# Optimization experiments

Measured on AMD Instinct MI355X. Metric: run time of the kernel, lower is better.

The kernel has to match this reference:

```python
import jax, jax.numpy as jnp
import numpy as np

B, N, D_FEAT = 16, 4096, 64
NPOINT, NSAMPLE = 1024, 32
MLP = [64, 64, 128]
IN_CH = 3 + D_FEAT
EPS = 1e-5  # BatchNorm eps (torch default)


def _fps(xyz, npoint):
    # Farthest point sampling; sequential scan over npoint steps (matches torch loop).
    b, n, _ = xyz.shape
    def step(carry, _):
        distance, farthest = carry  # (B,N) running min dist, (B,) current centroid idx
        centroid = jnp.take_along_axis(xyz, farthest[:, None, None], axis=1)  # (B,1,3)
        d = jnp.sum((xyz - centroid) ** 2, -1)  # (B,N)
        distance = jnp.minimum(distance, d)
        nxt = jnp.argmax(distance, -1).astype(jnp.int32)
        return (distance, nxt), farthest
    init = (jnp.full((b, n), jnp.inf, dtype=xyz.dtype),
            jnp.full((b,), n // 2, dtype=jnp.int32))
    _, centroids = jax.lax.scan(step, init, None, length=npoint)
    return centroids.T  # (B, npoint)


def _gather(pts, idx):
    # pts: (B,N,C); idx: (B,...) int -> (B,...,C)
    return jax.vmap(lambda p, i: p[i])(pts, idx)


def setup_inputs() -> dict:
    key = jax.random.key(0)
    ks = jax.random.split(key, 16)
    inp = {
        'xyz': jax.random.normal(ks[0], (B, N, 3), jnp.float32),
        'points': jax.random.normal(ks[1], (B, N, D_FEAT), jnp.float32),
    }
    last = IN_CH
    for li, oc in enumerate(MLP):
        inp[f'W{li}'] = jax.random.normal(ks[2 + li], (oc, last), jnp.float32) * (1.0 / np.sqrt(last))
        inp[f'b{li}'] = jnp.zeros((oc,), jnp.float32)
        inp[f'g{li}'] = jnp.ones((oc,), jnp.float32)
        inp[f'be{li}'] = jnp.zeros((oc,), jnp.float32)
        last = oc
    C = MLP[-1]; R = C // 8
    inp['aW1'] = jax.random.normal(ks[10], (R, C), jnp.float32) * (1.0 / np.sqrt(C))
    inp['aW2'] = jax.random.normal(ks[11], (C, R), jnp.float32) * (1.0 / np.sqrt(R))
    return inp


def reference(xyz, points, W0, b0, g0, be0, W1, b1, g1, be1, W2, b2, g2, be2, aW1, aW2):
    fps_idx = _fps(xyz, NPOINT)                 # (B,S) int32
    new_xyz = _gather(xyz, fps_idx)             # (B,S,3)
    # squared distances (B,S,N) via matmul expansion (as torch square_distance)
    d = (-2.0 * jnp.einsum('bsc,bnc->bsn', new_xyz, xyz)
         + jnp.sum(new_xyz ** 2, -1)[..., None]
         + jnp.sum(xyz ** 2, -1)[:, None, :])
    _, idx = jax.lax.top_k(-d, NSAMPLE)         # (B,S,k) nearest neighbors
    grouped_xyz = _gather(xyz, idx)             # (B,S,k,3)
    rel = grouped_xyz - new_xyz[:, :, None, :]  # relative coords
    feat = _gather(points, idx)                 # (B,S,k,D)
    g = jnp.concatenate([rel, feat], axis=-1)   # (B,S,k,3+D) channels-last
    # 1x1 conv MLP + BatchNorm (training-mode batch stats) + ReLU
    for (W, b, ga, be) in ((W0, b0, g0, be0), (W1, b1, g1, be1), (W2, b2, g2, be2)):
        g = jnp.einsum('bskc,oc->bsko', g, W) + b
        mu = g.mean(axis=(0, 1, 2))
        var = g.var(axis=(0, 1, 2))
        g = ga * (g - mu) * jax.lax.rsqrt(var + EPS) + be
        g = jax.nn.relu(g)
    new_points = g.max(axis=2)                  # max over nsample -> (B,S,C)
    # channel attention on (B,C,S) == reductions over S here
    avg = new_points.mean(axis=1)               # (B,C)
    mx = new_points.max(axis=1)                 # (B,C)
    def fc(v):
        return jnp.einsum('cr,br->bc', aW2, jax.nn.relu(jnp.einsum('rc,bc->br', aW1, v)))
    scale = jax.nn.sigmoid(fc(avg) + fc(mx))    # (B,C)
    new_points = new_points * scale[:, None, :]
    return new_xyz, new_points, fps_idx
```

## Files before the change

### kernel.cpp

```cpp
#include <hip/hip_runtime.h>
#include <hip/hip_bf16.h>

#define BB 16
#define NN 4096
#define SS 1024
#define KS 32
#define DF 64
#define INC 67
#define C1 64
#define C2 64
#define C3 128
#define ROWS (BB*SS*KS)
#define EPSBN 1e-5f
#define F_INF (__builtin_inff())

typedef __bf16 bf16;
typedef __bf16 bfrag __attribute__((ext_vector_type(8)));
typedef float  ffrag __attribute__((ext_vector_type(4)));
typedef float  f2    __attribute__((ext_vector_type(2)));
typedef unsigned long long u64;

#define OUT_NXYZ 0
#define OUT_NP   49152
#define OUT_FPS  2146304

#define OFF_FPS   0u
#define OFF_NXYZ  65536u
#define OFF_IDX   262144u
#define OFF_STATS 2359296u
#define OFF_ASUM  2555904u
#define OFF_AMAX  2621440u
#define OFF_BNC   2686976u
#define OFF_SCALE 2690048u
#define OFF_NP0   2698240u
#define OFF_YMAX  11086848u
#define OFF_H1    19475456u
#define OFF_H2    86584320u
#define ZERO_BYTES (196608u + 65536u + 65536u)

#define DPP_MAX_STEP(k, ctrl, rmask, bc) { \
  int _lo = __builtin_amdgcn_update_dpp(0, (int)(unsigned)(k), (ctrl), (rmask), 0xf, (bc)); \
  int _hi = __builtin_amdgcn_update_dpp(0, (int)((k)>>32),     (ctrl), (rmask), 0xf, (bc)); \
  u64 _k2 = ((u64)(unsigned)_hi << 32) | (unsigned)_lo; \
  if (_k2 > (k)) (k) = _k2; }

#define DPP_FMAX_STEP(v, ctrl, rmask, bc) { \
  int _t = __builtin_amdgcn_update_dpp(0, __float_as_int(v), (ctrl), (rmask), 0xf, (bc)); \
  (v) = fmaxf((v), __uint_as_float((unsigned)_t)); }

__device__ __forceinline__ u64 dpp_wavemax64(u64 k){
  DPP_MAX_STEP(k, 0x111, 0xf, true)
  DPP_MAX_STEP(k, 0x112, 0xf, true)
  DPP_MAX_STEP(k, 0x114, 0xf, true)
  DPP_MAX_STEP(k, 0x118, 0xf, true)
  DPP_MAX_STEP(k, 0x142, 0xa, false)
  DPP_MAX_STEP(k, 0x143, 0xc, false)
  return k;
}

__device__ __forceinline__ u64 readlane64(u64 k, int lane){
  unsigned lo = (unsigned)__builtin_amdgcn_readlane((int)(unsigned)k, lane);
  unsigned hi = (unsigned)__builtin_amdgcn_readlane((int)(k >> 32),   lane);
  return ((u64)hi << 32) | lo;
}

__device__ __forceinline__ u64 umax64(u64 a, u64 b){ return a > b ? a : b; }

__global__ __launch_bounds__(256) void fps_kernel(const float* __restrict__ xyz,
                                                  int* __restrict__ fps_i,
                                                  float* __restrict__ nxyz_ws,
                                                  float* __restrict__ out)
{
  #pragma clang fp contract(off)
  __shared__ __align__(16) float4 lc[NN];
  __shared__ int lfps[SS];
  __shared__ __align__(16) u64 slotk[2][4];
  int b = blockIdx.x, t = threadIdx.x;
  const float* xb = xyz + (size_t)b*NN*3;
  for (int p = t; p < NN; p += 256){
    lc[p] = make_float4(xb[p*3], xb[p*3+1], xb[p*3+2], 0.f);
  }
  __syncthreads();
  f2 px2[8], py2[8], pz2[8], pd2[8];
  int p0 = t*16;
  #pragma unroll
  for (int j=0;j<8;++j){
    float4 a = lc[p0+2*j], c = lc[p0+2*j+1];
    px2[j] = (f2){a.x, c.x}; py2[j] = (f2){a.y, c.y}; pz2[j] = (f2){a.z, c.z};
    pd2[j] = (f2){F_INF, F_INF};
  }
  float cx = lc[NN/2].x, cy = lc[NN/2].y, cz = lc[NN/2].z;
  if (t==0) lfps[0]=NN/2;
  int wv = t >> 6, lane = t & 63;
  for (int it=1; it<SS; ++it){
    f2 c2x = (f2){cx,cx}, c2y = (f2){cy,cy}, c2z = (f2){cz,cz};
    float bv=-1.f; int bi=p0;
    #pragma unroll
    for (int j=0;j<8;++j){
      f2 dx = px2[j]-c2x, dy = py2[j]-c2y, dz = pz2[j]-c2z;
      f2 d = (dx*dx + dy*dy) + dz*dz;
      f2 nd = (f2){fminf(pd2[j].x, d.x), fminf(pd2[j].y, d.y)};
      pd2[j]=nd;
      if (nd.x > bv){ bv=nd.x; bi=p0+2*j; }
      if (nd.y > bv){ bv=nd.y; bi=p0+2*j+1; }
    }
    float mv = bv;
    DPP_FMAX_STEP(mv, 0x111, 0xf, true)
    DPP_FMAX_STEP(mv, 0x112, 0xf, true)
    DPP_FMAX_STEP(mv, 0x114, 0xf, true)
    DPP_FMAX_STEP(mv, 0x118, 0xf, true)
    DPP_FMAX_STEP(mv, 0x142, 0xa, false)
    DPP_FMAX_STEP(mv, 0x143, 0xc, false)
    float wmax = __uint_as_float((unsigned)__builtin_amdgcn_readlane(__float_as_int(mv), 63));
    u64 em = __ballot(bv == wmax);
    int wl = (int)__builtin_ctzll(em);
    int wbi = __builtin_amdgcn_readlane(bi, wl);
    int p = it & 1;
    if (lane == 0)
      slotk[p][wv] = ((u64)__float_as_uint(wmax) << 32) | (unsigned)(~wbi);
    __syncthreads();
    ulonglong2 sA = *(const ulonglong2*)&slotk[p][0];
    ulonglong2 sB = *(const ulonglong2*)&slotk[p][2];
    u64 k = umax64(umax64(sA.x, sA.y), umax64(sB.x, sB.y));
    int i = ~(unsigned)k;
    float4 cc = lc[i];
    cx = cc.x; cy = cc.y; cz = cc.z;
    if (t==0) lfps[it]=i;
  }
  __syncthreads();
  for (int s=t; s<SS; s+=256){
    int i = lfps[s];
    fps_i[b*SS+s]=i;
    out[OUT_FPS + b*SS + s] = (float)i;
    float4 cc = lc[i];
    int o3 = (b*SS+s)*3;
    out[OUT_NXYZ+o3]=cc.x; out[OUT_NXYZ+o3+1]=cc.y; out[OUT_NXYZ+o3+2]=cc.z;
    nxyz_ws[o3]=cc.x; nxyz_ws[o3+1]=cc.y; nxyz_ws[o3+2]=cc.z;
  }
}

__global__ __launch_bounds__(64) void knn_kernel(const float* __restrict__ xyz,
                                                 const float* __restrict__ nxyz,
                                                 int* __restrict__ knn)
{
  __shared__ float ld[NN];
  int lane = threadIdx.x;
  int bs = blockIdx.x;
  int b = bs >> 10;
  const float* xb = xyz + (size_t)b*NN*3;
  float sx=nxyz[bs*3], sy=nxyz[bs*3+1], sz=nxyz[bs*3+2];
  float gv[8]; int gi[8];
  float lv = F_INF; int li = 0;
  #pragma unroll
  for (int g=0; g<8; ++g){
    float bgv = F_INF; int bgi = 0;
    #pragma unroll
    for (int jj=0; jj<8; ++jj){
      int p = (g*8+jj)*64 + lane;
      float dx=xb[p*3]-sx, dy=xb[p*3+1]-sy, dz=xb[p*3+2]-sz;
      float d = dx*dx+dy*dy+dz*dz;
      ld[p] = d;
      if (d < bgv){ bgv=d; bgi=p; }
    }
    gv[g]=bgv; gi[g]=bgi;
    if (bgv < lv){ lv=bgv; li=bgi; }
  }
  int kept = 0;
  for (int it=0; it<KS; ++it){
    u64 mk = ~(((u64)__float_as_uint(lv) << 32) | (unsigned)li);
    mk = dpp_wavemax64(mk);
    mk = readlane64(mk, 63);
    int i = (int)(unsigned)(~mk);
    if (lane==it) kept = i;
    if ((i & 63) == lane){
      int j = i >> 6;
      ld[i] = F_INF;
      int g = j >> 3;
      float bgv=F_INF; int bgi=0;
      for (int jj=0;jj<8;++jj){
        int p = (g*8+jj)*64 + lane;
        float d = ld[p];
        if (d<bgv){bgv=d;bgi=p;}
      }
      #pragma unroll
      for (int q=0;q<8;++q){ if (q==g){ gv[q]=bgv; gi[q]=bgi; } }
      lv=F_INF; li=0;
      #pragma unroll
      for (int q=0;q<8;++q){ if (gv[q]<lv){ lv=gv[q]; li=gi[q]; } }
    }
  }
  if (lane < KS) knn[bs*KS + lane] = kept;
}

__global__ __launch_bounds__(256) void conv1_kernel(const float* __restrict__ xyz,
                                                    const float* __restrict__ points,
                                                    const float* __restrict__ W0,
                                                    const float* __restrict__ b0,
                                                    const float* __restrict__ nxyz,
                                                    const int* __restrict__ knn,
                                                    bf16* __restrict__ h1,
                                                    float* __restrict__ stats)
{
  __shared__ __align__(16) bf16 As[64][104];
  __shared__ __align__(16) bf16 Bs[64][104];
  __shared__ float s1[C1], s2[C1];
  int t = threadIdx.x;
  int Rbase = blockIdx.x * 64;
  if (t < C1){ s1[t]=0.f; s2[t]=0.f; }
  {
    int o = t >> 2, q = t & 3;
    const float* wr = W0 + o*INC;
    for (int cc = q*24; cc < q*24+24; ++cc){
      float w;
      if (cc < 64) w = wr[3+cc];
      else if (cc < 67) w = wr[cc-64];
      else w = 0.f;
      Bs[o][cc] = (bf16)w;
    }
  }
  {
    int r = t >> 2, q = t & 3;
    int R = Rbase + r;
    int bs = R >> 5;
    int bIdx = bs >> 10;
    int nI = knn[R];
    const float* pr = points + ((size_t)(bIdx*NN + nI))*DF + q*16;
    float4 f0 = *(const float4*)(pr);
    float4 f1 = *(const float4*)(pr+4);
    float4 f2v = *(const float4*)(pr+8);
    float4 f3 = *(const float4*)(pr+12);
    bf16* ap = &As[r][q*16];
    ap[0]=(bf16)f0.x; ap[1]=(bf16)f0.y; ap[2]=(bf16)f0.z; ap[3]=(bf16)f0.w;
    ap[4]=(bf16)f1.x; ap[5]=(bf16)f1.y; ap[6]=(bf16)f1.z; ap[7]=(bf16)f1.w;
    ap[8]=(bf16)f2v.x; ap[9]=(bf16)f2v.y; ap[10]=(bf16)f2v.z; ap[11]=(bf16)f2v.w;
    ap[12]=(bf16)f3.x; ap[13]=(bf16)f3.y; ap[14]=(bf16)f3.z; ap[15]=(bf16)f3.w;
    if (q==0){
      const float* xr = xyz + ((size_t)(bIdx*NN + nI))*3;
      const float* nr = nxyz + bs*3;
      As[r][64]=(bf16)(xr[0]-nr[0]);
      As[r][65]=(bf16)(xr[1]-nr[1]);
      As[r][66]=(bf16)(xr[2]-nr[2]);
      for (int cc=67; cc<96; ++cc) As[r][cc]=(bf16)0.f;
    }
  }
  __syncthreads();
  int wv = t >> 6, lane = t & 63;
  int row16 = wv * 16;
  int arow = lane & 15, kgrp = lane >> 4;
  ffrag acc[4] = {};
  #pragma unroll
  for (int kc = 0; kc < 3; ++kc){
    bfrag af = *(const bfrag*)&As[row16 + arow][kc*32 + kgrp*8];
    #pragma unroll
    for (int nt = 0; nt < 4; ++nt){
      bfrag bfv = *(const bfrag*)&Bs[nt*16 + arow][kc*32 + kgrp*8];
      acc[nt] = __builtin_amdgcn_mfma_f32_16x16x32_bf16(af, bfv, acc[nt], 0,0,0);
    }
  }
  #pragma unroll
  for (int nt=0; nt<4; ++nt){
    int c = nt*16 + arow;
    float bias = b0[c];
    float ls1=0.f, ls2=0.f;
    #pragma unroll
    for (int r=0;r<4;++r){
      float y = acc[nt][r] + bias;
      int grow = Rbase + row16 + kgrp*4 + r;
      h1[(size_t)grow*C1 + c] = (bf16)y;
      ls1 += y; ls2 += y*y;
    }
    ls1 += __shfl_xor(ls1, 16); ls1 += __shfl_xor(ls1, 32);
    ls2 += __shfl_xor(ls2, 16); ls2 += __shfl_xor(ls2, 32);
    if (kgrp==0){ atomicAdd(&s1[c], ls1); atomicAdd(&s2[c], ls2); }
  }
  __syncthreads();
  if (t < C1){
    float* gp = stats + (blockIdx.x & 63)*256;
    atomicAdd(&gp[t], s1[t]);
    atomicAdd(&gp[128 + t], s2[t]);
  }
}

__global__ void bnfin_kernel(const float* __restrict__ stats, const float* __restrict__ g,
                             const float* __restrict__ be, float* __restrict__ bnc, int C)
{
  int c = threadIdx.x; if (c >= C) return;
  float a1=0.f, a2=0.f;
  for (int q=0;q<64;++q){ a1 += stats[q*256+c]; a2 += stats[q*256+128+c]; }
  float inv = 1.f/(float)ROWS;
  float mu = a1*inv; float var = a2*inv - mu*mu;
  float a = g[c]*rsqrtf(var + EPSBN);
  bnc[c] = a; bnc[128+c] = be[c] - mu*a;
}

__global__ __launch_bounds__(256) void conv2_kernel(const bf16* __restrict__ h1,
                                                    const float* __restrict__ W1,
                                                    const float* __restrict__ b1,
                                                    const float* __restrict__ bnc,
                                                    bf16* __restrict__ h2,
                                                    float* __restrict__ stats)
{
  __shared__ __align__(16) bf16 As[64][72];
  __shared__ __align__(16) bf16 Bs[64][72];
  __shared__ float s1[C2], s2[C2];
  int t = threadIdx.x;
  int Rbase = blockIdx.x * 64;
  if (t < C2){ s1[t]=0.f; s2[t]=0.f; }
  {
    int o = t >> 2, q = t & 3;
    const float* wr = W1 + o*64 + q*16;
    bf16* bp = &Bs[o][q*16];
    #pragma unroll
    for (int v=0; v<4; ++v){
      float4 f = *(const float4*)(wr + v*4);
      bp[v*4+0]=(bf16)f.x; bp[v*4+1]=(bf16)f.y; bp[v*4+2]=(bf16)f.z; bp[v*4+3]=(bf16)f.w;
    }
  }
  {
    int r = t >> 2, q = t & 3;
    int R = Rbase + r;
    const bf16* hr = h1 + (size_t)R*64 + q*16;
    bfrag h0 = *(const bfrag*)hr;
    bfrag h1v = *(const bfrag*)(hr+8);
    #pragma unroll
    for (int j=0;j<8;++j){
      int c=q*16+j;
      As[r][c] = (bf16)fmaxf(fmaf(bnc[c], (float)h0[j], bnc[128+c]), 0.f);
    }
    #pragma unroll
    for (int j=0;j<8;++j){
      int c=q*16+8+j;
      As[r][c] = (bf16)fmaxf(fmaf(bnc[c], (float)h1v[j], bnc[128+c]), 0.f);
    }
  }
  __syncthreads();
  int wv = t >> 6, lane = t & 63;
  int row16 = wv * 16;
  int arow = lane & 15, kgrp = lane >> 4;
  ffrag acc[4] = {};
  #pragma unroll
  for (int kc = 0; kc < 2; ++kc){
    bfrag af = *(const bfrag*)&As[row16 + arow][kc*32 + kgrp*8];
    #pragma unroll
    for (int nt = 0; nt < 4; ++nt){
      bfrag bfv = *(const bfrag*)&Bs[nt*16 + arow][kc*32 + kgrp*8];
      acc[nt] = __builtin_amdgcn_mfma_f32_16x16x32_bf16(af, bfv, acc[nt], 0,0,0);
    }
  }
  #pragma unroll
  for (int nt=0; nt<4; ++nt){
    int c = nt*16 + arow;
    float bias = b1[c];
    float ls1=0.f, ls2=0.f;
    #pragma unroll
    for (int r=0;r<4;++r){
      float y = acc[nt][r] + bias;
      int grow = Rbase + row16 + kgrp*4 + r;
      h2[(size_t)grow*C2 + c] = (bf16)y;
      ls1 += y; ls2 += y*y;
    }
    ls1 += __shfl_xor(ls1, 16); ls1 += __shfl_xor(ls1, 32);
    ls2 += __shfl_xor(ls2, 16); ls2 += __shfl_xor(ls2, 32);
    if (kgrp==0){ atomicAdd(&s1[c], ls1); atomicAdd(&s2[c], ls2); }
  }
  __syncthreads();
  if (t < C2){
    float* gp = stats + (blockIdx.x & 63)*256;
    atomicAdd(&gp[t], s1[t]);
    atomicAdd(&gp[128 + t], s2[t]);
  }
}

__global__ __launch_bounds__(256) void conv3_kernel(const bf16* __restrict__ h2,
                                                    const float* __restrict__ W2,
                                                    const float* __restrict__ b2,
                                                    const float* __restrict__ bnc,
                                                    float* __restrict__ ymax,
                                                    float* __restrict__ stats)
{
  __shared__ __align__(16) bf16 As[64][72];
  __shared__ __align__(16) bf16 Bs[128][72];
  __shared__ float s1[C3], s2[C3];
  __shared__ float wmax[4][C3];
  int t = threadIdx.x;
  int Rbase = blockIdx.x * 64;
  if (t < C3){ s1[t]=0.f; s2[t]=0.f; }
  {
    int o = t >> 1, q = t & 1;
    const float* wr = W2 + o*64 + q*32;
    bf16* bp = &Bs[o][q*32];
    #pragma unroll
    for (int v=0; v<8; ++v){
      float4 f = *(const float4*)(wr + v*4);
      bp[v*4+0]=(bf16)f.x; bp[v*4+1]=(bf16)f.y; bp[v*4+2]=(bf16)f.z; bp[v*4+3]=(bf16)f.w;
    }
  }
  {
    int r = t >> 2, q = t & 3;
    int R = Rbase + r;
    const bf16* hr = h2 + (size_t)R*64 + q*16;
    bfrag h0 = *(const bfrag*)hr;
    bfrag h1v = *(const bfrag*)(hr+8);
    #pragma unroll
    for (int j=0;j<8;++j){
      int c=q*16+j;
      As[r][c] = (bf16)fmaxf(fmaf(bnc[c], (float)h0[j], bnc[128+c]), 0.f);
    }
    #pragma unroll
    for (int j=0;j<8;++j){
      int c=q*16+8+j;
      As[r][c] = (bf16)fmaxf(fmaf(bnc[c], (float)h1v[j], bnc[128+c]), 0.f);
    }
  }
  __syncthreads();
  int wv = t >> 6, lane = t & 63;
  int row16 = wv * 16;
  int arow = lane & 15, kgrp = lane >> 4;
  ffrag acc[8] = {};
  #pragma unroll
  for (int kc = 0; kc < 2; ++kc){
    bfrag af = *(const bfrag*)&As[row16 + arow][kc*32 + kgrp*8];
    #pragma unroll
    for (int nt = 0; nt < 8; ++nt){
      bfrag bfv = *(const bfrag*)&Bs[nt*16 + arow][kc*32 + kgrp*8];
      acc[nt] = __builtin_amdgcn_mfma_f32_16x16x32_bf16(af, bfv, acc[nt], 0,0,0);
    }
  }
  #pragma unroll
  for (int nt=0; nt<8; ++nt){
    int c = nt*16 + arow;
    float bias = b2[c];
    float ls1=0.f, ls2=0.f, mm=-F_INF;
    #pragma unroll
    for (int r=0;r<4;++r){
      float y = acc[nt][r] + bias;
      ls1 += y; ls2 += y*y; mm = fmaxf(mm, y);
    }
    ls1 += __shfl_xor(ls1, 16); ls1 += __shfl_xor(ls1, 32);
    ls2 += __shfl_xor(ls2, 16); ls2 += __shfl_xor(ls2, 32);
    mm = fmaxf(mm, __shfl_xor(mm, 16)); mm = fmaxf(mm, __shfl_xor(mm, 32));
    if (kgrp==0){ atomicAdd(&s1[c], ls1); atomicAdd(&s2[c], ls2); wmax[wv][c]=mm; }
  }
  __syncthreads();
  {
    int half = t >> 7;
    int c = t & 127;
    float m = fmaxf(wmax[half*2][c], wmax[half*2+1][c]);
    ymax[(size_t)(blockIdx.x*2 + half)*C3 + c] = m;
  }
  if (t < C3){
    float* gp = stats + (blockIdx.x & 63)*256;
    atomicAdd(&gp[t], s1[t]);
    atomicAdd(&gp[128 + t], s2[t]);
  }
}

__global__ __launch_bounds__(256) void attreduce_kernel(const float* __restrict__ ymax,
                                                        const float* __restrict__ bnc,
                                                        float* __restrict__ np0,
                                                        float* __restrict__ asum,
                                                        unsigned* __restrict__ amax)
{
  __shared__ float rs[256], rm[256];
  int t = threadIdx.x;
  int b = blockIdx.x >> 3, sg = blockIdx.x & 7;
  int c = t & 127, h = t >> 7;
  float a = bnc[c], bb = bnc[128+c];
  size_t base = ((size_t)(b*1024 + sg*128 + h*64))*128 + c;
  float s = 0.f, m = 0.f;
  #pragma unroll 4
  for (int j=0;j<64;++j){
    float v = fmaxf(fmaf(a, ymax[base + (size_t)j*128], bb), 0.f);
    np0[base + (size_t)j*128] = v;
    s += v; m = fmaxf(m, v);
  }
  rs[t]=s; rm[t]=m;
  __syncthreads();
  if (t < 128){
    float s2 = rs[t] + rs[t+128];
    float m2 = fmaxf(rm[t], rm[t+128]);
    atomicAdd(&asum[b*128+t], s2);
    atomicMax(&amax[b*128+t], __float_as_uint(m2));
  }
}

__global__ __launch_bounds__(256) void attn_kernel(const float* __restrict__ asum,
                                                   const unsigned* __restrict__ amax,
                                                   const float* __restrict__ aW1,
                                                   const float* __restrict__ aW2,
                                                   float* __restrict__ scale)
{
  __shared__ float avg[16][128], mx[16][128], hA[16][16], hM[16][16];
  int t = threadIdx.x;
  for (int i=t; i<2048; i+=256){
    int b=i>>7, c=i&127;
    avg[b][c]=asum[i]*(1.f/1024.f); mx[b][c]=__uint_as_float(amax[i]);
  }
  __syncthreads();
  {
    int b=t>>4, r=t&15;
    float sa=0.f, sm=0.f;
    for (int c=0;c<128;++c){ float w=aW1[r*128+c]; sa+=w*avg[b][c]; sm+=w*mx[b][c]; }
    hA[b][r]=fmaxf(sa,0.f); hM[b][r]=fmaxf(sm,0.f);
  }
  __syncthreads();
  for (int i=t;i<2048;i+=256){
    int b=i>>7,c=i&127;
    float o=0.f;
    for (int r=0;r<16;++r){ o += aW2[c*16+r]*(hA[b][r]+hM[b][r]); }
    scale[i] = 1.f/(1.f+expf(-o));
  }
}

__global__ __launch_bounds__(256) void finout_kernel(const float* __restrict__ np0,
                                                     const float* __restrict__ scale,
                                                     float* __restrict__ out)
{
  int i = blockIdx.x*256 + threadIdx.x;
  int c = i & 127; int b = i >> 17;
  out[OUT_NP + i] = np0[i] * scale[b*128+c];
}

extern "C" void kernel_launch(void* const* d_in, const int* in_sizes, int n_in,
                              void* d_out, int out_size, void* d_ws, size_t ws_size,
                              hipStream_t stream)
{
  const float* xyz    = (const float*)d_in[0];
  const float* points = (const float*)d_in[1];
  const float* W0 = (const float*)d_in[2];
  const float* b0 = (const float*)d_in[3];
  const float* g0 = (const float*)d_in[4];
  const float* be0= (const float*)d_in[5];
  const float* W1 = (const float*)d_in[6];
  const float* b1 = (const float*)d_in[7];
  const float* g1 = (const float*)d_in[8];
  const float* be1= (const float*)d_in[9];
  const float* W2 = (const float*)d_in[10];
  const float* b2 = (const float*)d_in[11];
  const float* g2 = (const float*)d_in[12];
  const float* be2= (const float*)d_in[13];
  const float* aW1= (const float*)d_in[14];
  const float* aW2= (const float*)d_in[15];
  float* out = (float*)d_out;
  char* ws = (char*)d_ws;

  int*      fpsI  = (int*)(ws + OFF_FPS);
  float*    nxyz  = (float*)(ws + OFF_NXYZ);
  int*      knnI  = (int*)(ws + OFF_IDX);
  float*    stats = (float*)(ws + OFF_STATS);
  float*    asum  = (float*)(ws + OFF_ASUM);
  unsigned* amax  = (unsigned*)(ws + OFF_AMAX);
  float*    bnc   = (float*)(ws + OFF_BNC);
  float*    scl   = (float*)(ws + OFF_SCALE);
  float*    np0   = (float*)(ws + OFF_NP0);
  float*    ymax  = (float*)(ws + OFF_YMAX);
  bf16*     h1    = (bf16*)(ws + OFF_H1);
  bf16*     h2    = (bf16*)(ws + OFF_H2);

  hipMemsetAsync(ws + OFF_STATS, 0, ZERO_BYTES, stream);
  fps_kernel<<<BB, 256, 0, stream>>>(xyz, fpsI, nxyz, out);
  knn_kernel<<<BB*SS, 64, 0, stream>>>(xyz, nxyz, knnI);
  conv1_kernel<<<ROWS/64, 256, 0, stream>>>(xyz, points, W0, b0, nxyz, knnI, h1, stats);
  bnfin_kernel<<<1, 128, 0, stream>>>(stats, g0, be0, bnc, C1);
  conv2_kernel<<<ROWS/64, 256, 0, stream>>>(h1, W1, b1, bnc, h2, stats + 64*256);
  bnfin_kernel<<<1, 128, 0, stream>>>(stats + 64*256, g1, be1, bnc + 256, C2);
  conv3_kernel<<<ROWS/64, 256, 0, stream>>>(h2, W2, b2, bnc + 256, ymax, stats + 2*64*256);
  bnfin_kernel<<<1, 128, 0, stream>>>(stats + 2*64*256, g2, be2, bnc + 512, C3);
  attreduce_kernel<<<BB*8, 256, 0, stream>>>(ymax, bnc + 512, np0, asum, amax);
  attn_kernel<<<1, 256, 0, stream>>>(asum, amax, aW1, aW2, scl);
  finout_kernel<<<(BB*SS*C3)/256, 256, 0, stream>>>(np0, scl, out);
}
```

Baseline: 1.059 ms.

## Fuse BatchNorm finalize into consumer kernels and split FPS argmax chains

Removes the three single-block bnfin kernel launches. Each consumer block (conv2, conv3, attreduce) now reduces the 64 partial stat slots itself and computes the BN scale and shift into shared memory. Separately, the FPS inner argmax is split into two independent compare chains to shorten the serial dependency. The fusion saves launch gaps and tiny serial kernels, but each of the 4096 conv blocks now redundantly reads 64x2 stat values per channel, adding L2 traffic and a sync before its main work.

Result: no change. 1.051 ms (-0.7%).

```diff
diff --git a/kernel.cpp b/kernel.cpp
--- a/kernel.cpp
+++ b/kernel.cpp
@@ -94,16 +94,28 @@
   int wv = t >> 6, lane = t & 63;
   for (int it=1; it<SS; ++it){
     f2 c2x = (f2){cx,cx}, c2y = (f2){cy,cy}, c2z = (f2){cz,cz};
-    float bv=-1.f; int bi=p0;
-    #pragma unroll
-    for (int j=0;j<8;++j){
+    float bvA=-1.f; int biA=p0;
+    float bvB=-1.f; int biB=p0+8;
+    #pragma unroll
+    for (int j=0;j<4;++j){
       f2 dx = px2[j]-c2x, dy = py2[j]-c2y, dz = pz2[j]-c2z;
       f2 d = (dx*dx + dy*dy) + dz*dz;
       f2 nd = (f2){fminf(pd2[j].x, d.x), fminf(pd2[j].y, d.y)};
       pd2[j]=nd;
-      if (nd.x > bv){ bv=nd.x; bi=p0+2*j; }
-      if (nd.y > bv){ bv=nd.y; bi=p0+2*j+1; }
-    }
+      if (nd.x > bvA){ bvA=nd.x; biA=p0+2*j; }
+      if (nd.y > bvA){ bvA=nd.y; biA=p0+2*j+1; }
+    }
+    #pragma unroll
+    for (int j=4;j<8;++j){
+      f2 dx = px2[j]-c2x, dy = py2[j]-c2y, dz = pz2[j]-c2z;
+      f2 d = (dx*dx + dy*dy) + dz*dz;
+      f2 nd = (f2){fminf(pd2[j].x, d.x), fminf(pd2[j].y, d.y)};
+      pd2[j]=nd;
+      if (nd.x > bvB){ bvB=nd.x; biB=p0+2*j; }
+      if (nd.y > bvB){ bvB=nd.y; biB=p0+2*j+1; }
+    }
+    float bv = bvA; int bi = biA;
+    if (bvB > bvA){ bv = bvB; bi = biB; }
     float mv = bv;
     DPP_FMAX_STEP(mv, 0x111, 0xf, true)
     DPP_FMAX_STEP(mv, 0x112, 0xf, true)
@@ -281,31 +293,30 @@
   }
 }
 
-__global__ void bnfin_kernel(const float* __restrict__ stats, const float* __restrict__ g,
-                             const float* __restrict__ be, float* __restrict__ bnc, int C)
-{
-  int c = threadIdx.x; if (c >= C) return;
-  float a1=0.f, a2=0.f;
-  for (int q=0;q<64;++q){ a1 += stats[q*256+c]; a2 += stats[q*256+128+c]; }
-  float inv = 1.f/(float)ROWS;
-  float mu = a1*inv; float var = a2*inv - mu*mu;
-  float a = g[c]*rsqrtf(var + EPSBN);
-  bnc[c] = a; bnc[128+c] = be[c] - mu*a;
-}
-
 __global__ __launch_bounds__(256) void conv2_kernel(const bf16* __restrict__ h1,
                                                     const float* __restrict__ W1,
                                                     const float* __restrict__ b1,
-                                                    const float* __restrict__ bnc,
+                                                    const float* __restrict__ stats0,
+                                                    const float* __restrict__ g0,
+                                                    const float* __restrict__ be0,
                                                     bf16* __restrict__ h2,
                                                     float* __restrict__ stats)
 {
   __shared__ __align__(16) bf16 As[64][72];
   __shared__ __align__(16) bf16 Bs[64][72];
   __shared__ float s1[C2], s2[C2];
+  __shared__ float sbA[C2], sbB[C2];
   int t = threadIdx.x;
   int Rbase = blockIdx.x * 64;
   if (t < C2){ s1[t]=0.f; s2[t]=0.f; }
+  if (t < C2){
+    float a1=0.f, a2=0.f;
+    for (int q=0;q<64;++q){ a1 += stats0[q*256+t]; a2 += stats0[q*256+128+t]; }
+    float inv = 1.f/(float)ROWS;
+    float mu = a1*inv; float var = a2*inv - mu*mu;
+    float a = g0[t]*rsqrtf(var + EPSBN);
+    sbA[t] = a; sbB[t] = be0[t] - mu*a;
+  }
   {
     int o = t >> 2, q = t & 3;
     const float* wr = W1 + o*64 + q*16;
@@ -316,6 +327,7 @@
       bp[v*4+0]=(bf16)f.x; bp[v*4+1]=(bf16)f.y; bp[v*4+2]=(bf16)f.z; bp[v*4+3]=(bf16)f.w;
     }
   }
+  __syncthreads();
   {
     int r = t >> 2, q = t & 3;
     int R = Rbase + r;
@@ -325,12 +337,12 @@
     #pragma unroll
     for (int j=0;j<8;++j){
       int c=q*16+j;
-      As[r][c] = (bf16)fmaxf(fmaf(bnc[c], (float)h0[j], bnc[128+c]), 0.f);
+      As[r][c] = (bf16)fmaxf(fmaf(sbA[c], (float)h0[j], sbB[c]), 0.f);
     }
     #pragma unroll
     for (int j=0;j<8;++j){
       int c=q*16+8+j;
-      As[r][c] = (bf16)fmaxf(fmaf(bnc[c], (float)h1v[j], bnc[128+c]), 0.f);
+      As[r][c] = (bf16)fmaxf(fmaf(sbA[c], (float)h1v[j], sbB[c]), 0.f);
     }
   }
   __syncthreads();
@@ -374,7 +386,9 @@
 __global__ __launch_bounds__(256) void conv3_kernel(const bf16* __restrict__ h2,
                                                     const float* __restrict__ W2,
                                                     const float* __restrict__ b2,
-                                                    const float* __restrict__ bnc,
+                                                    const float* __restrict__ stats1,
+                                                    const float* __restrict__ g1,
+                                                    const float* __restrict__ be1,
                                                     float* __restrict__ ymax,
                                                     float* __restrict__ stats)
 {
@@ -382,9 +396,18 @@
   __shared__ __align__(16) bf16 Bs[128][72];
   __shared__ float s1[C3], s2[C3];
   __shared__ float wmax[4][C3];
+  __shared__ float sbA[C2], sbB[C2];
   int t = threadIdx.x;
   int Rbase = blockIdx.x * 64;
   if (t < C3){ s1[t]=0.f; s2[t]=0.f; }
+  if (t < C2){
+    float a1=0.f, a2=0.f;
+    for (int q=0;q<64;++q){ a1 += stats1[q*256+t]; a2 += stats1[q*256+128+t]; }
+    float inv = 1.f/(float)ROWS;
+    float mu = a1*inv; float var = a2*inv - mu*mu;
+    float a = g1[t]*rsqrtf(var + EPSBN);
+    sbA[t] = a; sbB[t] = be1[t] - mu*a;
+  }
   {
     int o = t >> 1, q = t & 1;
     const float* wr = W2 + o*64 + q*32;
@@ -395,6 +418,7 @@
       bp[v*4+0]=(bf16)f.x; bp[v*4+1]=(bf16)f.y; bp[v*4+2]=(bf16)f.z; bp[v*4+3]=(bf16)f.w;
     }
   }
+  __syncthreads();
   {
     int r = t >> 2, q = t & 3;
     int R = Rbase + r;
@@ -404,12 +428,12 @@
     #pragma unroll
     for (int j=0;j<8;++j){
       int c=q*16+j;
-      As[r][c] = (bf16)fmaxf(fmaf(bnc[c], (float)h0[j], bnc[128+c]), 0.f);
+      As[r][c] = (bf16)fmaxf(fmaf(sbA[c], (float)h0[j], sbB[c]), 0.f);
     }
     #pragma unroll
     for (int j=0;j<8;++j){
       int c=q*16+8+j;
-      As[r][c] = (bf16)fmaxf(fmaf(bnc[c], (float)h1v[j], bnc[128+c]), 0.f);
+      As[r][c] = (bf16)fmaxf(fmaf(sbA[c], (float)h1v[j], sbB[c]), 0.f);
     }
   }
   __syncthreads();
@@ -456,16 +480,28 @@
 }
 
 __global__ __launch_bounds__(256) void attreduce_kernel(const float* __restrict__ ymax,
-                                                        const float* __restrict__ bnc,
+                                                        const float* __restrict__ stats2,
+                                                        const float* __restrict__ g2,
+                                                        const float* __restrict__ be2,
                                                         float* __restrict__ np0,
                                                         float* __restrict__ asum,
                                                         unsigned* __restrict__ amax)
 {
   __shared__ float rs[256], rm[256];
+  __shared__ float sbA[C3], sbB[C3];
   int t = threadIdx.x;
+  if (t < C3){
+    float a1=0.f, a2=0.f;
+    for (int q=0;q<64;++q){ a1 += stats2[q*256+t]; a2 += stats2[q*256+128+t]; }
+    float inv = 1.f/(float)ROWS;
+    float mu = a1*inv; float var = a2*inv - mu*mu;
+    float a = g2[t]*rsqrtf(var + EPSBN);
+    sbA[t] = a; sbB[t] = be2[t] - mu*a;
+  }
+  __syncthreads();
   int b = blockIdx.x >> 3, sg = blockIdx.x & 7;
   int c = t & 127, h = t >> 7;
-  float a = bnc[c], bb = bnc[128+c];
+  float a = sbA[c], bb = sbB[c];
   size_t base = ((size_t)(b*1024 + sg*128 + h*64))*128 + c;
   float s = 0.f, m = 0.f;
   #pragma unroll 4
@@ -550,7 +586,6 @@
   float*    stats = (float*)(ws + OFF_STATS);
   float*    asum  = (float*)(ws + OFF_ASUM);
   unsigned* amax  = (unsigned*)(ws + OFF_AMAX);
-  float*    bnc   = (float*)(ws + OFF_BNC);
   float*    scl   = (float*)(ws + OFF_SCALE);
   float*    np0   = (float*)(ws + OFF_NP0);
   float*    ymax  = (float*)(ws + OFF_YMAX);
@@ -561,12 +596,9 @@
   fps_kernel<<<BB, 256, 0, stream>>>(xyz, fpsI, nxyz, out);
   knn_kernel<<<BB*SS, 64, 0, stream>>>(xyz, nxyz, knnI);
   conv1_kernel<<<ROWS/64, 256, 0, stream>>>(xyz, points, W0, b0, nxyz, knnI, h1, stats);
-  bnfin_kernel<<<1, 128, 0, stream>>>(stats, g0, be0, bnc, C1);
-  conv2_kernel<<<ROWS/64, 256, 0, stream>>>(h1, W1, b1, bnc, h2, stats + 64*256);
-  bnfin_kernel<<<1, 128, 0, stream>>>(stats + 64*256, g1, be1, bnc + 256, C2);
-  conv3_kernel<<<ROWS/64, 256, 0, stream>>>(h2, W2, b2, bnc + 256, ymax, stats + 2*64*256);
-  bnfin_kernel<<<1, 128, 0, stream>>>(stats + 2*64*256, g2, be2, bnc + 512, C3);
-  attreduce_kernel<<<BB*8, 256, 0, stream>>>(ymax, bnc + 512, np0, asum, amax);
+  conv2_kernel<<<ROWS/64, 256, 0, stream>>>(h1, W1, b1, stats, g0, be0, h2, stats + 64*256);
+  conv3_kernel<<<ROWS/64, 256, 0, stream>>>(h2, W2, b2, stats + 64*256, g1, be1, ymax, stats + 2*64*256);
+  attreduce_kernel<<<BB*8, 256, 0, stream>>>(ymax, stats + 2*64*256, g2, be2, np0, asum, amax);
   attn_kernel<<<1, 256, 0, stream>>>(asum, amax, aW1, aW2, scl);
   finout_kernel<<<(BB*SS*C3)/256, 256, 0, stream>>>(np0, scl, out);
 }
```
